# Performance work log

Measured on AMD Instinct MI355X. Metric: run time of the kernel, lower is better.

The kernel has to match this reference:

```python
import jax, jax.numpy as jnp
import numpy as np

NUM_HEADS = 32
ROPE_BASE = 10000.0
MASK_NEG = -66504.0  # from (1 - tril) * -66504.0 in the source


def _rotate_half(x):
    d = x.shape[-1] // 2
    return jnp.concatenate([-x[..., d:], x[..., :d]], axis=-1)


def setup_inputs() -> dict:
    key = jax.random.key(0)
    k1, k2, k3, k4 = jax.random.split(key, 4)
    S, B, E = 2048, 2, 2048
    return {
        "hidden_states": jax.random.normal(k1, (S, B, E), dtype=jnp.float32) * 0.02,
        "qkv_w": jax.random.normal(k2, (E, 3 * E), dtype=jnp.float32) * 0.02,
        "qkv_b": jax.random.normal(k3, (3 * E,), dtype=jnp.float32) * 0.02,
        "out_w": jax.random.normal(k4, (E, E), dtype=jnp.float32) * 0.02,
        "out_b": jnp.zeros((E,), dtype=jnp.float32),
    }


def reference(hidden_states, qkv_w, qkv_b, out_w, out_b):
    # seq-first prompt/prefill path of IPEXTransformerAtten
    S, B, E = hidden_states.shape
    H = NUM_HEADS
    D = E // H

    # fused QKV projection (mm_qkv_out)
    qkv = jnp.einsum('sbe,ef->sbf', hidden_states, qkv_w) + qkv_b  # [S,B,3E]
    q, k, v = jnp.split(qkv, 3, axis=-1)
    q = q.reshape(S, B, H, D)
    k = k.reshape(S, B, H, D)
    v = v.reshape(S, B, H, D)

    # rotary embedding (GPT-NeoX style, full head_dim)
    inv_freq = 1.0 / (ROPE_BASE ** (jnp.arange(0, D, 2, dtype=jnp.float32) / D))
    freqs = jnp.arange(S, dtype=jnp.float32)[:, None] * inv_freq  # [S, D/2]
    emb = jnp.concatenate([freqs, freqs], axis=-1)  # [S, D]
    cos = jnp.cos(emb)[:, None, None, :].astype(hidden_states.dtype)
    sin = jnp.sin(emb)[:, None, None, :].astype(hidden_states.dtype)
    q = q * cos + _rotate_half(q) * sin
    k = k * cos + _rotate_half(k) * sin

    # scaled dot-product attention with causal mask
    scale = 1.0 / jnp.sqrt(jnp.array(D, dtype=hidden_states.dtype))
    scores = jnp.einsum('sbhd,tbhd->bhst', q, k) * scale  # [B,H,S,S]
    causal = jnp.tril(jnp.ones((S, S), dtype=scores.dtype))
    scores = scores + (1.0 - causal) * MASK_NEG
    attn = jax.nn.softmax(scores, axis=-1)
    ctx = jnp.einsum('bhst,tbhd->sbhd', attn, v).reshape(S, B, E)

    # output projection
    return jnp.einsum('sbe,ef->sbf', ctx, out_w) + out_b
```

## Files before the change

kernel.cpp:

```cpp
#include <hip/hip_runtime.h>
#include <hip/hip_bf16.h>

#define S_LEN 2048
#define BATCH 2
#define EMB   2048
#define NH    32
#define HD    64
#define M_ROWS (S_LEN * BATCH)
#define QKV_N  (3 * EMB)

typedef short bf16x8 __attribute__((ext_vector_type(8)));
typedef float f32x4  __attribute__((ext_vector_type(4)));

__device__ __forceinline__ unsigned short f2bf(float f) {
  unsigned int u = __float_as_uint(f);
  u += 0x7fffu + ((u >> 16) & 1u);
  return (unsigned short)(u >> 16);
}
__device__ __forceinline__ float bf2f(unsigned short h) {
  return __uint_as_float(((unsigned int)h) << 16);
}
__device__ __forceinline__ void async_copy16(const void* g, void* lds_d) {
  __builtin_amdgcn_global_load_lds(
      (const __attribute__((address_space(1))) void*)g,
      (__attribute__((address_space(3))) void*)lds_d, 16, 0, 0);
}

#if __has_builtin(__builtin_amdgcn_exp2f)
#define EXP2F(x) __builtin_amdgcn_exp2f(x)
#else
#define EXP2F(x) __expf((x) * 0.6931471805599453f)
#endif


#define CAST_BLKS  (M_ROWS * EMB / 4 / 256)
#define TCQ_BX     (QKV_N / 64)
#define TCQ_BLKS   (TCQ_BX * (EMB / 64))
#define TCO_BX     (EMB / 64)
#define TCO_BLKS   (TCO_BX * (EMB / 64))
#define PREP_BLKS  (CAST_BLKS + TCQ_BLKS + TCO_BLKS)

__device__ __forceinline__ void transpose_body(
    const float* __restrict__ in, unsigned short* __restrict__ out,
    int R, int C, int bx, int by, int tid) {
  __shared__ unsigned short t[64][65];
  const int bc = bx * 64, br = by * 64;
  const int tx = tid & 63, ty = tid >> 6;
  #pragma unroll
  for (int rr = ty; rr < 64; rr += 4)
    t[rr][tx] = f2bf(in[(size_t)(br + rr) * C + bc + tx]);
  __syncthreads();
  #pragma unroll
  for (int rr = ty; rr < 64; rr += 4)
    out[(size_t)(bc + rr) * R + br + tx] = t[tx][rr];
}

__global__ __launch_bounds__(256) void prep_all(
    const float* __restrict__ hidden, unsigned short* __restrict__ hbf,
    const float* __restrict__ qkv_w, unsigned short* __restrict__ qkvwT,
    const float* __restrict__ out_w, unsigned short* __restrict__ outwT) {
  const int bid = blockIdx.x, tid = threadIdx.x;
  if (bid < CAST_BLKS) {
    const int i = bid * 256 + tid;
    float4 v = reinterpret_cast<const float4*>(hidden)[i];
    ushort4 o;
    o.x = f2bf(v.x); o.y = f2bf(v.y); o.z = f2bf(v.z); o.w = f2bf(v.w);
    reinterpret_cast<ushort4*>(hbf)[i] = o;
  } else if (bid < CAST_BLKS + TCQ_BLKS) {
    const int b = bid - CAST_BLKS;
    transpose_body(qkv_w, qkvwT, EMB, QKV_N, b % TCQ_BX, b / TCQ_BX, tid);
  } else {
    const int b = bid - CAST_BLKS - TCQ_BLKS;
    transpose_body(out_w, outwT, EMB, EMB, b % TCO_BX, b / TCO_BX, tid);
  }
}


constexpr int TILE_SH = 24576;
constexpr int GEMM_LDS_BYTES = 3 * TILE_SH * 2;

__global__ __launch_bounds__(512, 2) void gemm_qkv(
    const unsigned short* __restrict__ A,
    const unsigned short* __restrict__ Wt,
    const float* __restrict__ bias,
    unsigned short* __restrict__ Qo,
    unsigned short* __restrict__ Ko,
    unsigned short* __restrict__ VTo) {
  extern __shared__ unsigned short lds[];
  const int tid = threadIdx.x;
  const int n0 = blockIdx.x * 128;
  const int m0 = blockIdx.y * 256;
  const int wave = tid >> 6, lane = tid & 63;
  const int wm = (wave >> 1) * 64, wn = (wave & 1) * 64;
  const int lm = lane & 15, lq = lane >> 4;
  const int K = 2048;
  const int NT = K / 64;

  const int srow = tid >> 3;
  const int gch  = (tid & 7) ^ (srow & 7);
  const unsigned short* Ab = A  + (size_t)(m0 + srow) * K + gch * 8;
  const unsigned short* Bb = Wt + (size_t)(n0 + srow) * K + gch * 8;

  auto stA = [&](int bufi, int k0, int rep) {
    async_copy16(Ab + (size_t)rep * 64 * K + k0,
                 lds + (size_t)bufi * TILE_SH + ((size_t)rep * 512 + tid) * 8);
  };
  auto stB = [&](int bufi, int k0, int rep) {
    async_copy16(Bb + (size_t)rep * 64 * K + k0,
                 lds + (size_t)bufi * TILE_SH + 16384 + ((size_t)rep * 512 + tid) * 8);
  };

  f32x4 acc[4][4] = {};

  stA(0, 0, 0); stA(0, 0, 1); stA(0, 0, 2); stA(0, 0, 3); stB(0, 0, 0); stB(0, 0, 1);
  stA(1, 64, 0); stA(1, 64, 1); stA(1, 64, 2); stA(1, 64, 3); stB(1, 64, 0); stB(1, 64, 1);
  asm volatile("s_waitcnt vmcnt(6)" ::: "memory");
  __builtin_amdgcn_s_barrier();

  int cur = 0;
  for (int t = 0; t < NT; t++) {
    const unsigned short* Abuf = lds + (size_t)cur * TILE_SH;
    const unsigned short* Bbuf = Abuf + 16384;
    const int pb = (cur >= 1) ? cur - 1 : 2;
    const int pk = (t + 2) * 64;
    const bool pre = (t + 2) < NT;

    bf16x8 b[4][2], a[2][2];
    #pragma unroll
    for (int j = 0; j < 4; j++) {
      const int R = wn + j * 16 + lm;
      #pragma unroll
      for (int ks = 0; ks < 2; ks++)
        b[j][ks] = *reinterpret_cast<const bf16x8*>(
            Bbuf + (size_t)R * 64 + (((ks * 4 + lq) ^ (R & 7)) * 8));
    }
    #pragma unroll
    for (int i = 0; i < 2; i++) {
      const int R = wm + i * 16 + lm;
      #pragma unroll
      for (int ks = 0; ks < 2; ks++)
        a[i][ks] = *reinterpret_cast<const bf16x8*>(
            Abuf + (size_t)R * 64 + (((ks * 4 + lq) ^ (R & 7)) * 8));
    }
    if (pre) { stA(pb, pk, 0); stA(pb, pk, 1); stB(pb, pk, 0); }
    __builtin_amdgcn_s_barrier();
    asm volatile("s_waitcnt lgkmcnt(0)" ::: "memory");
    __builtin_amdgcn_s_setprio(1);
    #pragma unroll
    for (int ks = 0; ks < 2; ks++)
      #pragma unroll
      for (int i = 0; i < 2; i++)
        #pragma unroll
        for (int j = 0; j < 4; j++)
          acc[i][j] = __builtin_amdgcn_mfma_f32_16x16x32_bf16(a[i][ks], b[j][ks], acc[i][j], 0, 0, 0);
    __builtin_amdgcn_s_setprio(0);
    __builtin_amdgcn_s_barrier();

    #pragma unroll
    for (int i = 0; i < 2; i++) {
      const int R = wm + (i + 2) * 16 + lm;
      #pragma unroll
      for (int ks = 0; ks < 2; ks++)
        a[i][ks] = *reinterpret_cast<const bf16x8*>(
            Abuf + (size_t)R * 64 + (((ks * 4 + lq) ^ (R & 7)) * 8));
    }
    if (pre) { stA(pb, pk, 2); stA(pb, pk, 3); stB(pb, pk, 1); }
    __builtin_amdgcn_s_barrier();
    asm volatile("s_waitcnt lgkmcnt(0)" ::: "memory");
    __builtin_amdgcn_s_setprio(1);
    #pragma unroll
    for (int ks = 0; ks < 2; ks++)
      #pragma unroll
      for (int i = 0; i < 2; i++)
        #pragma unroll
        for (int j = 0; j < 4; j++)
          acc[i + 2][j] = __builtin_amdgcn_mfma_f32_16x16x32_bf16(a[i][ks], b[j][ks], acc[i + 2][j], 0, 0, 0);
    __builtin_amdgcn_s_setprio(0);
    if (t + 1 < NT) {
      if (pre) asm volatile("s_waitcnt vmcnt(6)" ::: "memory");
      else     asm volatile("s_waitcnt vmcnt(0)" ::: "memory");
      __builtin_amdgcn_s_barrier();
    }
    cur = (cur == 2) ? 0 : cur + 1;
  }

  const int which = n0 >> 11;
  float bv[4];
  #pragma unroll
  for (int j = 0; j < 4; j++) bv[j] = bias[n0 + wn + j * 16 + lm];

  if (which < 2) {
    unsigned short* dst = (which == 0) ? Qo : Ko;
    #pragma unroll
    for (int j = 0; j < 2; j++) {
      const int n = n0 + wn + j * 16 + lm;
      const int e = n & (EMB - 1), h = e >> 6, d = e & 63;
      const float invf = EXP2F((float)d * -0.4152410118609203f);
      #pragma unroll
      for (int i = 0; i < 4; i++) {
        #pragma unroll
        for (int r = 0; r < 4; r++) {
          const int m = m0 + wm + i * 16 + lq * 4 + r;
          const int s = m >> 1, b = m & 1;
          const float v1 = acc[i][j][r]     + bv[j];
          const float v2 = acc[i][j + 2][r] + bv[j + 2];
          float sn, cs;
          __sincosf((float)s * invf, &sn, &cs);
          const size_t base = (((size_t)b * NH + h) * S_LEN + s) * HD + d;
          dst[base]      = f2bf(v1 * cs - v2 * sn);
          dst[base + 32] = f2bf(v2 * cs + v1 * sn);
        }
      }
    }
  } else {
    __syncthreads();
    unsigned short* T = lds;
    #pragma unroll
    for (int j = 0; j < 4; j++) {
      const int nl = wn + j * 16 + lm;
      #pragma unroll
      for (int i = 0; i < 4; i++) {
        const int sbase = (wm >> 1) + i * 8 + lq * 2;
        #pragma unroll
        for (int r = 0; r < 4; r++)
          T[nl * 264 + (r & 1) * 128 + sbase + (r >> 1)] = f2bf(acc[i][j][r] + bv[j]);
      }
    }
    __syncthreads();
    const int h0 = (n0 & (EMB - 1)) >> 6;
    const int s0 = m0 >> 1;
    #pragma unroll
    for (int k = 0; k < 8; k++) {
      const int c = k * 512 + tid;
      const int row = c >> 4, ch = c & 15;
      const int nl = row >> 1, bb = row & 1;
      const bf16x8 v = *reinterpret_cast<const bf16x8*>(T + nl * 264 + bb * 128 + ch * 8);
      const int hh = h0 + (nl >> 6), d = nl & 63;
      *reinterpret_cast<bf16x8*>(
          VTo + (((size_t)bb * NH + hh) * HD + d) * S_LEN + s0 + ch * 8) = v;
    }
  }
}


__global__ __launch_bounds__(256) void attn_kernel(
    const unsigned short* __restrict__ Q,
    const unsigned short* __restrict__ K,
    const unsigned short* __restrict__ VT,
    unsigned short* __restrict__ ctx) {
  const int bh = blockIdx.x;
  const int p  = blockIdx.y;
  const int tid = threadIdx.x;
  const int wave = tid >> 6, lane = tid & 63;
  const int lm = lane & 15, lq = lane >> 4;
  const int b = bh >> 5, h = bh & 31;
  const char* Qb8 = (const char*)(Q  + (size_t)bh * S_LEN * HD);
  const char* Kb8 = (const char*)(K  + (size_t)bh * S_LEN * HD);
  const char* Vb8 = (const char*)(VT + (size_t)bh * HD * S_LEN);

  __shared__ __align__(16) unsigned short Ks[2][2][64][32];
  __shared__ __align__(16) unsigned short Vs[2][2][64][32];
  __shared__ __align__(16) unsigned short Pbuf[4][32][72];
  unsigned short* Pw = &Pbuf[wave][0][0];

  const float C = 0.18033688011112042f;
  const int q0A = p * 128, q0B = (15 - p) * 128;
  const int r0A = q0A + wave * 32, r0B = q0B + wave * 32;
  const int nt = (q0B >> 6) + 2;

  const int srw = tid >> 2, sc16 = (tid & 3) * 16;

  bf16x8 qf[2][2][2];
  #pragma unroll
  for (int s = 0; s < 2; s++) {
    const int rr = (s == 0) ? r0A : r0B;
    #pragma unroll
    for (int i = 0; i < 2; i++)
      #pragma unroll
      for (int ks = 0; ks < 2; ks++)
        qf[s][i][ks] = *reinterpret_cast<const bf16x8*>(
            Qb8 + (size_t)(rr + i*16 + lm) * 128 + ks*64 + lq*16);
  }

  f32x4 O[2][2][4] = {};
  float l[2][2][4] = {};

  {
    char* kd = (char*)&Ks[0][0][0][0];
    char* vd = (char*)&Vs[0][0][0][0];
    async_copy16(Kb8 + (size_t)srw * 128      + sc16, kd        + tid*16);
    async_copy16(Kb8 + (size_t)srw * 128 + 64 + sc16, kd + 4096 + tid*16);
    async_copy16(Vb8 + (size_t)srw * 4096      + sc16, vd        + tid*16);
    async_copy16(Vb8 + (size_t)srw * 4096 + 64 + sc16, vd + 4096 + tid*16);
  }
  __syncthreads();

  for (int t = 0; t < nt; t++) {
    const int t0 = t * 64;
    const int buf = t & 1;

    if (t + 1 < nt) {
      const int t1 = t0 + 64;
      char* kd = (char*)&Ks[buf ^ 1][0][0][0];
      char* vd = (char*)&Vs[buf ^ 1][0][0][0];
      async_copy16(Kb8 + (size_t)(t1 + srw) * 128      + sc16, kd        + tid*16);
      async_copy16(Kb8 + (size_t)(t1 + srw) * 128 + 64 + sc16, kd + 4096 + tid*16);
      async_copy16(Vb8 + (size_t)srw * 4096 + t1*2      + sc16, vd        + tid*16);
      async_copy16(Vb8 + (size_t)srw * 4096 + t1*2 + 64 + sc16, vd + 4096 + tid*16);
    }

    const char* KsB = (const char*)&Ks[buf][0][0][0];
    const char* VsB = (const char*)&Vs[buf][0][0][0];

    #pragma unroll
    for (int s = 0; s < 2; s++) {
      const int rr = (s == 0) ? r0A : r0B;
      if (t0 <= rr + 31) {
        const bool clean = (t0 + 63 <= rr);
        const int jmax  = clean ? 4 : ((rr == t0) ? 2 : 4);
        const int kslim = clean ? 2 : ((rr == t0) ? 1 : 2);
        const int srow_c = rr + lq * 4;

        f32x4 sc[2][4] = {};
        #pragma unroll
        for (int ks = 0; ks < 2; ks++) {
          bf16x8 kf[4];
          #pragma unroll
          for (int j = 0; j < 4; j++)
            if (j < jmax)
              kf[j] = *reinterpret_cast<const bf16x8*>(
                  KsB + ks*4096 + (j*16 + lm)*64 + lq*16);
          #pragma unroll
          for (int i = 0; i < 2; i++)
            #pragma unroll
            for (int j = 0; j < 4; j++)
              if (j < jmax)
                sc[i][j] = __builtin_amdgcn_mfma_f32_16x16x32_bf16(
                    qf[s][i][ks], kf[j], sc[i][j], 0, 0, 0);
        }

        if (clean) {
          #pragma unroll
          for (int i = 0; i < 2; i++)
            #pragma unroll
            for (int j = 0; j < 4; j++)
              #pragma unroll
              for (int r = 0; r < 4; r++) {
                const float pe = EXP2F(sc[i][j][r] * C);
                l[s][i][r] += pe;
                Pw[(i*16 + lq*4 + r) * 72 + j*16 + lm] = f2bf(pe);
              }
        } else {
          #pragma unroll
          for (int i = 0; i < 2; i++)
            #pragma unroll
            for (int j = 0; j < 4; j++)
              if (j < jmax)
                #pragma unroll
                for (int r = 0; r < 4; r++) {
                  const int srow = srow_c + i*16 + r;
                  const int tcol = t0 + j*16 + lm;
                  const float pe = (tcol <= srow) ? EXP2F(sc[i][j][r] * C) : 0.0f;
                  l[s][i][r] += pe;
                  Pw[(i*16 + lq*4 + r) * 72 + j*16 + lm] = f2bf(pe);
                }
        }

        #pragma unroll
        for (int ks = 0; ks < 2; ks++) {
          if (ks < kslim) {
            bf16x8 pf[2], vf[4];
            #pragma unroll
            for (int i = 0; i < 2; i++)
              pf[i] = *reinterpret_cast<const bf16x8*>(Pw + (i*16 + lm)*72 + ks*32 + lq*8);
            #pragma unroll
            for (int j = 0; j < 4; j++)
              vf[j] = *reinterpret_cast<const bf16x8*>(
                  VsB + ks*4096 + (j*16 + lm)*64 + lq*16);
            #pragma unroll
            for (int i = 0; i < 2; i++)
              #pragma unroll
              for (int j = 0; j < 4; j++)
                O[s][i][j] = __builtin_amdgcn_mfma_f32_16x16x32_bf16(
                    pf[i], vf[j], O[s][i][j], 0, 0, 0);
          }
        }
      }
    }
    __syncthreads();
  }

  #pragma unroll
  for (int s = 0; s < 2; s++) {
    const int rr = (s == 0) ? r0A : r0B;
    #pragma unroll
    for (int i = 0; i < 2; i++) {
      #pragma unroll
      for (int r = 0; r < 4; r++) {
        float sum = l[s][i][r];
        sum += __shfl_xor(sum, 1, 64);
        sum += __shfl_xor(sum, 2, 64);
        sum += __shfl_xor(sum, 4, 64);
        sum += __shfl_xor(sum, 8, 64);
        const float inv = 1.0f / sum;
        const int srow = rr + lq*4 + i*16 + r;
        #pragma unroll
        for (int j = 0; j < 4; j++) {
          const int d = j*16 + lm;
          ctx[((size_t)srow * BATCH + b) * EMB + h*HD + d] = f2bf(O[s][i][j][r] * inv);
        }
      }
    }
  }
}


__global__ __launch_bounds__(512, 2) void gemm_out(
    const unsigned short* __restrict__ A,
    const unsigned short* __restrict__ Wt,
    const float* __restrict__ bias,
    float* __restrict__ out) {
  extern __shared__ unsigned short lds[];
  const int tid = threadIdx.x;
  const int n0 = blockIdx.x * 128;
  const int m0 = blockIdx.y * 256;
  const int wave = tid >> 6, lane = tid & 63;
  const int wm = (wave >> 1) * 64, wn = (wave & 1) * 64;
  const int lm = lane & 15, lq = lane >> 4;
  const int K = 2048;
  const int NT = K / 64;

  const int srow = tid >> 3;
  const int gch  = (tid & 7) ^ (srow & 7);
  const unsigned short* Ab = A  + (size_t)(m0 + srow) * K + gch * 8;
  const unsigned short* Bb = Wt + (size_t)(n0 + srow) * K + gch * 8;

  auto stA = [&](int bufi, int k0, int rep) {
    async_copy16(Ab + (size_t)rep * 64 * K + k0,
                 lds + (size_t)bufi * TILE_SH + ((size_t)rep * 512 + tid) * 8);
  };
  auto stB = [&](int bufi, int k0, int rep) {
    async_copy16(Bb + (size_t)rep * 64 * K + k0,
                 lds + (size_t)bufi * TILE_SH + 16384 + ((size_t)rep * 512 + tid) * 8);
  };

  f32x4 acc[4][4] = {};

  stA(0, 0, 0); stA(0, 0, 1); stA(0, 0, 2); stA(0, 0, 3); stB(0, 0, 0); stB(0, 0, 1);
  stA(1, 64, 0); stA(1, 64, 1); stA(1, 64, 2); stA(1, 64, 3); stB(1, 64, 0); stB(1, 64, 1);
  asm volatile("s_waitcnt vmcnt(6)" ::: "memory");
  __builtin_amdgcn_s_barrier();

  int cur = 0;
  for (int t = 0; t < NT; t++) {
    const unsigned short* Abuf = lds + (size_t)cur * TILE_SH;
    const unsigned short* Bbuf = Abuf + 16384;
    const int pb = (cur >= 1) ? cur - 1 : 2;
    const int pk = (t + 2) * 64;
    const bool pre = (t + 2) < NT;

    bf16x8 b[4][2], a[2][2];
    #pragma unroll
    for (int j = 0; j < 4; j++) {
      const int R = wn + j * 16 + lm;
      #pragma unroll
      for (int ks = 0; ks < 2; ks++)
        b[j][ks] = *reinterpret_cast<const bf16x8*>(
            Bbuf + (size_t)R * 64 + (((ks * 4 + lq) ^ (R & 7)) * 8));
    }
    #pragma unroll
    for (int i = 0; i < 2; i++) {
      const int R = wm + i * 16 + lm;
      #pragma unroll
      for (int ks = 0; ks < 2; ks++)
        a[i][ks] = *reinterpret_cast<const bf16x8*>(
            Abuf + (size_t)R * 64 + (((ks * 4 + lq) ^ (R & 7)) * 8));
    }
    if (pre) { stA(pb, pk, 0); stA(pb, pk, 1); stB(pb, pk, 0); }
    __builtin_amdgcn_s_barrier();
    asm volatile("s_waitcnt lgkmcnt(0)" ::: "memory");
    __builtin_amdgcn_s_setprio(1);
    #pragma unroll
    for (int ks = 0; ks < 2; ks++)
      #pragma unroll
      for (int i = 0; i < 2; i++)
        #pragma unroll
        for (int j = 0; j < 4; j++)
          acc[i][j] = __builtin_amdgcn_mfma_f32_16x16x32_bf16(a[i][ks], b[j][ks], acc[i][j], 0, 0, 0);
    __builtin_amdgcn_s_setprio(0);
    __builtin_amdgcn_s_barrier();

    #pragma unroll
    for (int i = 0; i < 2; i++) {
      const int R = wm + (i + 2) * 16 + lm;
      #pragma unroll
      for (int ks = 0; ks < 2; ks++)
        a[i][ks] = *reinterpret_cast<const bf16x8*>(
            Abuf + (size_t)R * 64 + (((ks * 4 + lq) ^ (R & 7)) * 8));
    }
    if (pre) { stA(pb, pk, 2); stA(pb, pk, 3); stB(pb, pk, 1); }
    __builtin_amdgcn_s_barrier();
    asm volatile("s_waitcnt lgkmcnt(0)" ::: "memory");
    __builtin_amdgcn_s_setprio(1);
    #pragma unroll
    for (int ks = 0; ks < 2; ks++)
      #pragma unroll
      for (int i = 0; i < 2; i++)
        #pragma unroll
        for (int j = 0; j < 4; j++)
          acc[i + 2][j] = __builtin_amdgcn_mfma_f32_16x16x32_bf16(a[i][ks], b[j][ks], acc[i + 2][j], 0, 0, 0);
    __builtin_amdgcn_s_setprio(0);
    if (t + 1 < NT) {
      if (pre) asm volatile("s_waitcnt vmcnt(6)" ::: "memory");
      else     asm volatile("s_waitcnt vmcnt(0)" ::: "memory");
      __builtin_amdgcn_s_barrier();
    }
    cur = (cur == 2) ? 0 : cur + 1;
  }

  #pragma unroll
  for (int j = 0; j < 4; j++) {
    const int n = n0 + wn + j * 16 + lm;
    const float bv = bias[n];
    #pragma unroll
    for (int i = 0; i < 4; i++) {
      #pragma unroll
      for (int r = 0; r < 4; r++) {
        const int m = m0 + wm + i * 16 + lq * 4 + r;
        out[(size_t)m * EMB + n] = acc[i][j][r] + bv;
      }
    }
  }
}


extern "C" void kernel_launch(void* const* d_in, const int* in_sizes, int n_in,
                              void* d_out, int out_size, void* d_ws, size_t ws_size,
                              hipStream_t stream) {
  const float* hidden = (const float*)d_in[0];
  const float* qkv_w  = (const float*)d_in[1];
  const float* qkv_b  = (const float*)d_in[2];
  const float* out_w  = (const float*)d_in[3];
  const float* out_b  = (const float*)d_in[4];
  float* out = (float*)d_out;

  static bool attr_set = false;
  if (!attr_set) {
    hipFuncSetAttribute(reinterpret_cast<const void*>(gemm_qkv),
                        hipFuncAttributeMaxDynamicSharedMemorySize, GEMM_LDS_BYTES);
    hipFuncSetAttribute(reinterpret_cast<const void*>(gemm_out),
                        hipFuncAttributeMaxDynamicSharedMemorySize, GEMM_LDS_BYTES);
    attr_set = true;
  }

  unsigned short* ws = (unsigned short*)d_ws;
  unsigned short* hbf   = ws;
  unsigned short* qkvwT = hbf   + (size_t)M_ROWS * EMB;
  unsigned short* outwT = qkvwT + (size_t)QKV_N * EMB;
  unsigned short* Qb    = outwT + (size_t)EMB * EMB;
  unsigned short* Kb    = Qb    + (size_t)64 * S_LEN * HD;
  unsigned short* VTb   = Kb    + (size_t)64 * S_LEN * HD;
  unsigned short* ctx   = VTb   + (size_t)64 * S_LEN * HD;

  prep_all<<<PREP_BLKS, 256, 0, stream>>>(hidden, hbf, qkv_w, qkvwT, out_w, outwT);

  gemm_qkv<<<dim3(QKV_N / 128, M_ROWS / 256), 512, GEMM_LDS_BYTES, stream>>>(
      hbf, qkvwT, qkv_b, Qb, Kb, VTb);

  attn_kernel<<<dim3(64, 8), 256, 0, stream>>>(Qb, Kb, VTb, ctx);

  gemm_out<<<dim3(EMB / 128, M_ROWS / 256), 512, GEMM_LDS_BYTES, stream>>>(
      ctx, outwT, out_b, out);
}
```

Measured before the change: 361.1 us.

## Compute transposed scores and pass P to PV MFMA via shuffles instead of LDS

```diff
diff --git a/kernel.cpp b/kernel.cpp
--- a/kernel.cpp
+++ b/kernel.cpp
@@ -11,11 +11,15 @@
 
 typedef short bf16x8 __attribute__((ext_vector_type(8)));
 typedef float f32x4  __attribute__((ext_vector_type(4)));
+typedef unsigned int u32x4 __attribute__((ext_vector_type(4)));
 
 __device__ __forceinline__ unsigned short f2bf(float f) {
   unsigned int u = __float_as_uint(f);
   u += 0x7fffu + ((u >> 16) & 1u);
   return (unsigned short)(u >> 16);
+}
+__device__ __forceinline__ unsigned int pk2(float a, float b) {
+  return (unsigned int)f2bf(a) | ((unsigned int)f2bf(b) << 16);
 }
 __device__ __forceinline__ float bf2f(unsigned short h) {
   return __uint_as_float(((unsigned int)h) << 16);
@@ -243,7 +247,7 @@
 }
 
 
-__global__ __launch_bounds__(256) void attn_kernel(
+__global__ __launch_bounds__(256, 3) void attn_kernel(
     const unsigned short* __restrict__ Q,
     const unsigned short* __restrict__ K,
     const unsigned short* __restrict__ VT,
@@ -260,8 +264,6 @@
 
   __shared__ __align__(16) unsigned short Ks[2][2][64][32];
   __shared__ __align__(16) unsigned short Vs[2][2][64][32];
-  __shared__ __align__(16) unsigned short Pbuf[4][32][72];
-  unsigned short* Pw = &Pbuf[wave][0][0];
 
   const float C = 0.18033688011112042f;
   const int q0A = p * 128, q0B = (15 - p) * 128;
@@ -269,6 +271,7 @@
   const int nt = (q0B >> 6) + 2;
 
   const int srw = tid >> 2, sc16 = (tid & 3) * 16;
+  const int src0 = lm + ((lane & 16) << 1);
 
   bf16x8 qf[2][2][2];
   #pragma unroll
@@ -283,7 +286,7 @@
   }
 
   f32x4 O[2][2][4] = {};
-  float l[2][2][4] = {};
+  float l[2][2] = {};
 
   {
     char* kd = (char*)&Ks[0][0][0][0];
@@ -319,7 +322,6 @@
         const bool clean = (t0 + 63 <= rr);
         const int jmax  = clean ? 4 : ((rr == t0) ? 2 : 4);
         const int kslim = clean ? 2 : ((rr == t0) ? 1 : 2);
-        const int srow_c = rr + lq * 4;
 
         f32x4 sc[2][4] = {};
         #pragma unroll
@@ -336,53 +338,68 @@
             for (int j = 0; j < 4; j++)
               if (j < jmax)
                 sc[i][j] = __builtin_amdgcn_mfma_f32_16x16x32_bf16(
-                    qf[s][i][ks], kf[j], sc[i][j], 0, 0, 0);
+                    kf[j], qf[s][i][ks], sc[i][j], 0, 0, 0);
         }
 
+        unsigned int W[2][4][2];
         if (clean) {
           #pragma unroll
           for (int i = 0; i < 2; i++)
             #pragma unroll
-            for (int j = 0; j < 4; j++)
-              #pragma unroll
-              for (int r = 0; r < 4; r++) {
-                const float pe = EXP2F(sc[i][j][r] * C);
-                l[s][i][r] += pe;
-                Pw[(i*16 + lq*4 + r) * 72 + j*16 + lm] = f2bf(pe);
-              }
+            for (int j = 0; j < 4; j++) {
+              const float p0 = EXP2F(sc[i][j][0] * C);
+              const float p1 = EXP2F(sc[i][j][1] * C);
+              const float p2 = EXP2F(sc[i][j][2] * C);
+              const float p3 = EXP2F(sc[i][j][3] * C);
+              l[s][i] += (p0 + p1) + (p2 + p3);
+              W[i][j][0] = pk2(p0, p1);
+              W[i][j][1] = pk2(p2, p3);
+            }
         } else {
           #pragma unroll
-          for (int i = 0; i < 2; i++)
+          for (int i = 0; i < 2; i++) {
+            const int qr = rr + i*16 + lm;
             #pragma unroll
             for (int j = 0; j < 4; j++)
-              if (j < jmax)
+              if (j < jmax) {
+                const int kb = t0 + j*16 + lq*4;
+                float pe[4];
                 #pragma unroll
                 for (int r = 0; r < 4; r++) {
-                  const int srow = srow_c + i*16 + r;
-                  const int tcol = t0 + j*16 + lm;
-                  const float pe = (tcol <= srow) ? EXP2F(sc[i][j][r] * C) : 0.0f;
-                  l[s][i][r] += pe;
-                  Pw[(i*16 + lq*4 + r) * 72 + j*16 + lm] = f2bf(pe);
+                  pe[r] = (kb + r <= qr) ? EXP2F(sc[i][j][r] * C) : 0.0f;
+                  l[s][i] += pe[r];
                 }
+                W[i][j][0] = pk2(pe[0], pe[1]);
+                W[i][j][1] = pk2(pe[2], pe[3]);
+              }
+          }
         }
 
         #pragma unroll
         for (int ks = 0; ks < 2; ks++) {
           if (ks < kslim) {
-            bf16x8 pf[2], vf[4];
-            #pragma unroll
-            for (int i = 0; i < 2; i++)
-              pf[i] = *reinterpret_cast<const bf16x8*>(Pw + (i*16 + lm)*72 + ks*32 + lq*8);
+            bf16x8 vf[4];
             #pragma unroll
             for (int j = 0; j < 4; j++)
               vf[j] = *reinterpret_cast<const bf16x8*>(
                   VsB + ks*4096 + (j*16 + lm)*64 + lq*16);
             #pragma unroll
-            for (int i = 0; i < 2; i++)
+            for (int i = 0; i < 2; i++) {
+              unsigned int w[4];
+              #pragma unroll
+              for (int m = 0; m < 4; m++) {
+                const int srcl = src0 + (m >> 1) * 16;
+                const unsigned int ta = (unsigned int)__shfl((int)W[i][ks*2][m & 1], srcl, 64);
+                const unsigned int tb = (unsigned int)__shfl((int)W[i][ks*2 + 1][m & 1], srcl, 64);
+                w[m] = (lq & 2) ? tb : ta;
+              }
+              const u32x4 pu = {w[0], w[1], w[2], w[3]};
+              const bf16x8 pf = __builtin_bit_cast(bf16x8, pu);
               #pragma unroll
               for (int j = 0; j < 4; j++)
                 O[s][i][j] = __builtin_amdgcn_mfma_f32_16x16x32_bf16(
-                    pf[i], vf[j], O[s][i][j], 0, 0, 0);
+                    pf, vf[j], O[s][i][j], 0, 0, 0);
+            }
           }
         }
       }
@@ -395,15 +412,13 @@
     const int rr = (s == 0) ? r0A : r0B;
     #pragma unroll
     for (int i = 0; i < 2; i++) {
+      float lv = l[s][i];
+      lv += __shfl_xor(lv, 16, 64);
+      lv += __shfl_xor(lv, 32, 64);
       #pragma unroll
       for (int r = 0; r < 4; r++) {
-        float sum = l[s][i][r];
-        sum += __shfl_xor(sum, 1, 64);
-        sum += __shfl_xor(sum, 2, 64);
-        sum += __shfl_xor(sum, 4, 64);
-        sum += __shfl_xor(sum, 8, 64);
-        const float inv = 1.0f / sum;
-        const int srow = rr + lq*4 + i*16 + r;
+        const float inv = 1.0f / __shfl(lv, lq*4 + r, 64);
+        const int srow = rr + i*16 + lq*4 + r;
         #pragma unroll
         for (int j = 0; j < 4; j++) {
           const int d = j*16 + lm;
```

Measured after the change: 403.0 us. 11.6% more time.

## Halve attention query tile per block and double grid for more parallelism

Applied to the files above, without the earlier changes.

```diff
diff --git a/kernel.cpp b/kernel.cpp
--- a/kernel.cpp
+++ b/kernel.cpp
@@ -243,7 +243,7 @@
 }
 
 
-__global__ __launch_bounds__(256) void attn_kernel(
+__global__ __launch_bounds__(256, 3) void attn_kernel(
     const unsigned short* __restrict__ Q,
     const unsigned short* __restrict__ K,
     const unsigned short* __restrict__ VT,
@@ -260,30 +260,28 @@
 
   __shared__ __align__(16) unsigned short Ks[2][2][64][32];
   __shared__ __align__(16) unsigned short Vs[2][2][64][32];
-  __shared__ __align__(16) unsigned short Pbuf[4][32][72];
+  __shared__ __align__(16) unsigned short Pbuf[4][16][72];
   unsigned short* Pw = &Pbuf[wave][0][0];
 
   const float C = 0.18033688011112042f;
-  const int q0A = p * 128, q0B = (15 - p) * 128;
-  const int r0A = q0A + wave * 32, r0B = q0B + wave * 32;
-  const int nt = (q0B >> 6) + 2;
+  const int q0A = p * 64, q0B = (31 - p) * 64;
+  const int r0A = q0A + wave * 16, r0B = q0B + wave * 16;
+  const int nt = (q0B >> 6) + 1;
 
   const int srw = tid >> 2, sc16 = (tid & 3) * 16;
 
-  bf16x8 qf[2][2][2];
+  bf16x8 qf[2][2];
   #pragma unroll
   for (int s = 0; s < 2; s++) {
     const int rr = (s == 0) ? r0A : r0B;
     #pragma unroll
-    for (int i = 0; i < 2; i++)
-      #pragma unroll
-      for (int ks = 0; ks < 2; ks++)
-        qf[s][i][ks] = *reinterpret_cast<const bf16x8*>(
-            Qb8 + (size_t)(rr + i*16 + lm) * 128 + ks*64 + lq*16);
-  }
-
-  f32x4 O[2][2][4] = {};
-  float l[2][2][4] = {};
+    for (int ks = 0; ks < 2; ks++)
+      qf[s][ks] = *reinterpret_cast<const bf16x8*>(
+          Qb8 + (size_t)(rr + lm) * 128 + ks*64 + lq*16);
+  }
+
+  f32x4 O[2][4] = {};
+  float l[2][4] = {};
 
   {
     char* kd = (char*)&Ks[0][0][0][0];
@@ -315,13 +313,13 @@
     #pragma unroll
     for (int s = 0; s < 2; s++) {
       const int rr = (s == 0) ? r0A : r0B;
-      if (t0 <= rr + 31) {
+      if (t0 <= rr + 15) {
         const bool clean = (t0 + 63 <= rr);
-        const int jmax  = clean ? 4 : ((rr == t0) ? 2 : 4);
-        const int kslim = clean ? 2 : ((rr == t0) ? 1 : 2);
-        const int srow_c = rr + lq * 4;
-
-        f32x4 sc[2][4] = {};
+        const int d4 = clean ? 3 : ((rr - t0) >> 4);
+        const int jmax  = clean ? 4 : (d4 + 1);
+        const int kslim = clean ? 2 : ((d4 >> 1) + 1);
+
+        f32x4 sc[4] = {};
         #pragma unroll
         for (int ks = 0; ks < 2; ks++) {
           bf16x8 kf[4];
@@ -331,58 +329,51 @@
               kf[j] = *reinterpret_cast<const bf16x8*>(
                   KsB + ks*4096 + (j*16 + lm)*64 + lq*16);
           #pragma unroll
-          for (int i = 0; i < 2; i++)
-            #pragma unroll
-            for (int j = 0; j < 4; j++)
-              if (j < jmax)
-                sc[i][j] = __builtin_amdgcn_mfma_f32_16x16x32_bf16(
-                    qf[s][i][ks], kf[j], sc[i][j], 0, 0, 0);
+          for (int j = 0; j < 4; j++)
+            if (j < jmax)
+              sc[j] = __builtin_amdgcn_mfma_f32_16x16x32_bf16(
+                  qf[s][ks], kf[j], sc[j], 0, 0, 0);
         }
 
         if (clean) {
           #pragma unroll
-          for (int i = 0; i < 2; i++)
+          for (int j = 0; j < 4; j++)
             #pragma unroll
-            for (int j = 0; j < 4; j++)
+            for (int r = 0; r < 4; r++) {
+              const float pe = EXP2F(sc[j][r] * C);
+              l[s][r] += pe;
+              Pw[(lq*4 + r) * 72 + j*16 + lm] = f2bf(pe);
+            }
+        } else {
+          const int srow_c = rr + lq * 4;
+          const int jwrite = kslim * 2;
+          #pragma unroll
+          for (int j = 0; j < 4; j++)
+            if (j < jwrite)
               #pragma unroll
               for (int r = 0; r < 4; r++) {
-                const float pe = EXP2F(sc[i][j][r] * C);
-                l[s][i][r] += pe;
-                Pw[(i*16 + lq*4 + r) * 72 + j*16 + lm] = f2bf(pe);
+                const int srow = srow_c + r;
+                const int tcol = t0 + j*16 + lm;
+                const float pe = (tcol <= srow) ? EXP2F(sc[j][r] * C) : 0.0f;
+                l[s][r] += pe;
+                Pw[(lq*4 + r) * 72 + j*16 + lm] = f2bf(pe);
               }
-        } else {
-          #pragma unroll
-          for (int i = 0; i < 2; i++)
-            #pragma unroll
-            for (int j = 0; j < 4; j++)
-              if (j < jmax)
-                #pragma unroll
-                for (int r = 0; r < 4; r++) {
-                  const int srow = srow_c + i*16 + r;
-                  const int tcol = t0 + j*16 + lm;
-                  const float pe = (tcol <= srow) ? EXP2F(sc[i][j][r] * C) : 0.0f;
-                  l[s][i][r] += pe;
-                  Pw[(i*16 + lq*4 + r) * 72 + j*16 + lm] = f2bf(pe);
-                }
         }
 
         #pragma unroll
         for (int ks = 0; ks < 2; ks++) {
           if (ks < kslim) {
-            bf16x8 pf[2], vf[4];
-            #pragma unroll
-            for (int i = 0; i < 2; i++)
-              pf[i] = *reinterpret_cast<const bf16x8*>(Pw + (i*16 + lm)*72 + ks*32 + lq*8);
+            bf16x8 vf[4];
+            const bf16x8 pf = *reinterpret_cast<const bf16x8*>(
+                Pw + lm*72 + ks*32 + lq*8);
             #pragma unroll
             for (int j = 0; j < 4; j++)
               vf[j] = *reinterpret_cast<const bf16x8*>(
                   VsB + ks*4096 + (j*16 + lm)*64 + lq*16);
             #pragma unroll
-            for (int i = 0; i < 2; i++)
-              #pragma unroll
-              for (int j = 0; j < 4; j++)
-                O[s][i][j] = __builtin_amdgcn_mfma_f32_16x16x32_bf16(
-                    pf[i], vf[j], O[s][i][j], 0, 0, 0);
+            for (int j = 0; j < 4; j++)
+              O[s][j] = __builtin_amdgcn_mfma_f32_16x16x32_bf16(
+                  pf, vf[j], O[s][j], 0, 0, 0);
           }
         }
       }
@@ -394,21 +385,18 @@
   for (int s = 0; s < 2; s++) {
     const int rr = (s == 0) ? r0A : r0B;
     #pragma unroll
-    for (int i = 0; i < 2; i++) {
-      #pragma unroll
-      for (int r = 0; r < 4; r++) {
-        float sum = l[s][i][r];
-        sum += __shfl_xor(sum, 1, 64);
-        sum += __shfl_xor(sum, 2, 64);
-        sum += __shfl_xor(sum, 4, 64);
-        sum += __shfl_xor(sum, 8, 64);
-        const float inv = 1.0f / sum;
-        const int srow = rr + lq*4 + i*16 + r;
-        #pragma unroll
-        for (int j = 0; j < 4; j++) {
-          const int d = j*16 + lm;
-          ctx[((size_t)srow * BATCH + b) * EMB + h*HD + d] = f2bf(O[s][i][j][r] * inv);
-        }
+    for (int r = 0; r < 4; r++) {
+      float sum = l[s][r];
+      sum += __shfl_xor(sum, 1, 64);
+      sum += __shfl_xor(sum, 2, 64);
+      sum += __shfl_xor(sum, 4, 64);
+      sum += __shfl_xor(sum, 8, 64);
+      const float inv = 1.0f / sum;
+      const int srow = rr + lq*4 + r;
+      #pragma unroll
+      for (int j = 0; j < 4; j++) {
+        const int d = j*16 + lm;
+        ctx[((size_t)srow * BATCH + b) * EMB + h*HD + d] = f2bf(O[s][j][r] * inv);
       }
     }
   }
@@ -567,7 +555,7 @@
   gemm_qkv<<<dim3(QKV_N / 128, M_ROWS / 256), 512, GEMM_LDS_BYTES, stream>>>(
       hbf, qkvwT, qkv_b, Qb, Kb, VTb);
 
-  attn_kernel<<<dim3(64, 8), 256, 0, stream>>>(Qb, Kb, VTb, ctx);
+  attn_kernel<<<dim3(64, 16), 256, 0, stream>>>(Qb, Kb, VTb, ctx);
 
   gemm_out<<<dim3(EMB / 128, M_ROWS / 256), 512, GEMM_LDS_BYTES, stream>>>(
       ctx, outwT, out_b, out);
```

Measured after the change: 396.3 us. 9.7% more time.
